# Performance work log

Hardware: AMD Instinct MI355X
Metric: run time of the kernel (lower is better)

The kernel has to match this reference:

```python
import jax, jax.numpy as jnp
import numpy as np

BN_EPS = 1e-5
N_EULER = 8


def _bn_train(x, gamma, beta):
    # BatchNorm1d in training mode: biased batch statistics over the batch axis
    mu = jnp.mean(x, axis=0)
    var = jnp.mean((x - mu) ** 2, axis=0)
    return gamma * (x - mu) / jnp.sqrt(var + BN_EPS) + beta


def setup_inputs() -> dict:
    key = jax.random.key(0)
    ks = jax.random.split(key, 16)
    B, d, u_dim, n_obs, sdim = 4096, 512, 64, 25, 128
    h1, h2, hd = 1024, 1024, 512

    def w(k, shape, fan_in):
        return jax.random.normal(k, shape, dtype=jnp.float32) / np.sqrt(fan_in)

    return {
        "z_dyn": jax.random.normal(ks[0], (B, d), dtype=jnp.float32),
        "z_static": jax.random.normal(ks[1], (B, sdim), dtype=jnp.float32),
        "dt": jnp.array(0.05, dtype=jnp.float32),
        "ut": jax.random.normal(ks[2], (B, u_dim), dtype=jnp.float32),
        "eps": jax.random.normal(ks[3], (N_EULER, B, d), dtype=jnp.float32),
        "W1": w(ks[4], (h1, d), d), "b1": jnp.zeros((h1,), jnp.float32),
        "g1": jnp.ones((h1,), jnp.float32), "be1": jnp.zeros((h1,), jnp.float32),
        "W2": w(ks[5], (h2, h1), h1), "b2": jnp.zeros((h2,), jnp.float32),
        "g2": jnp.ones((h2,), jnp.float32), "be2": jnp.zeros((h2,), jnp.float32),
        "W3": w(ks[6], (d, h2), h2), "b3": jnp.zeros((d,), jnp.float32),
        "Wd1": w(ks[7], (hd, d), d), "bd1": jnp.zeros((hd,), jnp.float32),
        "Wd2": w(ks[8], (d, hd), hd), "bd2": jnp.zeros((d,), jnp.float32),
        "B_sde": w(ks[9], (d, u_dim), u_dim),
        "C": w(ks[10], (n_obs, d), d),
        "D": w(ks[11], (n_obs, u_dim), u_dim),
    }


def reference(z_dyn, z_static, dt, ut, eps,
              W1, b1, g1, be1, W2, b2, g2, be2, W3, b3,
              Wd1, bd1, Wd2, bd2, B_sde, C, D):
    h = dt / N_EULER
    sqrt_h = jnp.sqrt(jnp.abs(h) + 1e-8)

    def drift(z):
        a = jax.nn.relu(_bn_train(z @ W1.T + b1, g1, be1))
        a = jax.nn.relu(_bn_train(a @ W2.T + b2, g2, be2))
        return a @ W3.T + b3

    def diffusion(z):
        t = jnp.tanh(z @ Wd1.T + bd1)
        return jax.nn.softplus(t @ Wd2.T + bd2) + 1e-5

    def step(z, e):
        f = drift(z)
        g = diffusion(z)
        z = z + h * f + sqrt_h * g * e  # Euler-Maruyama update (training mode)
        return z, None

    z, _ = jax.lax.scan(step, z_dyn, eps)
    ut_dt = ut * dt
    z_next = z + ut_dt @ B_sde.T
    yt = z_next @ C.T + ut_dt @ D.T
    return (z_next, yt)
```

## Files before the change

### kernel.cpp

```cpp
#include <hip/hip_runtime.h>


typedef unsigned short ushort_t;
typedef __bf16 bf16x8 __attribute__((ext_vector_type(8)));
typedef float f32x4 __attribute__((ext_vector_type(4)));

__device__ __forceinline__ float bf2f(ushort_t s) {
  unsigned u = ((unsigned)s) << 16;
  return __uint_as_float(u);
}
__device__ __forceinline__ ushort_t f2bf(float f) {
  unsigned u = __float_as_uint(f);
  unsigned lsb = (u >> 16) & 1u;
  u += 0x7fffu + lsb;
  return (ushort_t)(u >> 16);
}
__device__ __forceinline__ float ldin(const void* p, size_t i, int f32) {
  return f32 ? ((const float*)p)[i] : bf2f(((const ushort_t*)p)[i]);
}
__device__ __forceinline__ void async16(const void* g, void* l) {
  __builtin_amdgcn_global_load_lds(
      (const __attribute__((address_space(1))) void*)g,
      (__attribute__((address_space(3))) void*)l, 16, 0, 0);
}

__global__ void k_detect(const void* __restrict__ eps, const void* __restrict__ dtraw,
                         float* __restrict__ consts) {
  __shared__ float mx[256];
  const int t = threadIdx.x;
  const ushort_t* e = (const ushort_t*)eps;
  float m = 0.f;
#pragma unroll
  for (int k = 0; k < 4; ++k) {
    float v = fabsf(bf2f(e[t * 4 + k]));
    if (!(v < 1e30f)) v = 1e30f;
    m = fmaxf(m, v);
  }
  mx[t] = m;
  __syncthreads();
  if (t == 0) {
    float M = 0.f;
    for (int k = 0; k < 256; ++k) M = fmaxf(M, mx[k]);
    const int f32 = (M > 1e3f) ? 1 : 0;
    float dt;
    if (f32) {
      dt = *(const float*)dtraw;
    } else {
      float db = bf2f(*(const ushort_t*)dtraw);
      float df = *(const float*)dtraw;
      dt = (db > 1e-6f && db < 1e3f) ? db : df;
    }
    const float h = dt * 0.125f;
    consts[0] = h;
    consts[1] = sqrtf(fabsf(h) + 1e-8f);
    consts[2] = dt;
    consts[3] = (float)f32;
  }
}

struct ConvArgs { const void* src[5]; };
#define CONV_TOT 2621440

__global__ void k_conv(ConvArgs a, const float* __restrict__ consts,
                       ushort_t* __restrict__ base) {
  constexpr int CUM[6] = {0, 524288, 786432, 1835008, 2359296, 2621440};
  const int f32 = consts[3] != 0.f;
  const int i = (blockIdx.x * 256 + threadIdx.x) * 4;
  if (i >= CONV_TOT) return;
  int j = 0;
#pragma unroll
  for (int k = 1; k < 5; ++k)
    if (i >= CUM[k]) j = k;
  const int local = i - CUM[j];
  const void* s = a.src[j];
  ushort4 o;
  if (f32) {
    float4 v = ((const float4*)s)[local >> 2];
    o = make_ushort4(f2bf(v.x), f2bf(v.y), f2bf(v.z), f2bf(v.w));
  } else {
    o = ((const ushort4*)s)[local >> 2];
  }
  *(ushort4*)(base + i) = o;
}

template <int MT, int MODE, int STATS, int FUSE, int BIAS, int FINAL, int ANORM>
__device__ __forceinline__ void gemm_body(
    const ushort_t* __restrict__ A, const ushort_t* __restrict__ W,
    const void* __restrict__ bias, int ncol0, ushort_t* __restrict__ Cout,
    int Nout, int K, int m0, int n0, __bf16* As, __bf16* Bs,
    float* __restrict__ s1, float* __restrict__ s2,
    const ushort_t* __restrict__ Gb, float* __restrict__ zf,
    ushort_t* __restrict__ zb, const void* __restrict__ eps,
    unsigned long long eoff, const float* __restrict__ consts,
    const float* __restrict__ Ub, float* __restrict__ out0,
    const float* __restrict__ s1in, const float* __restrict__ s2in,
    const void* __restrict__ gsc, const void* __restrict__ gbe,
    float* scF, float* shF) {
  constexpr int BM = MT * 64;
  const int f32 = consts[3] != 0.f;
  const int tid = threadIdx.x;
  const int lane = tid & 63;
  const int wave = tid >> 6;
  const int col = lane & 15;
  const int quad = lane >> 4;
  const int rowBase = wave * (BM / 4);

  if (ANORM) {
    const float inv = 1.0f / 4096.0f;
    for (int c = tid; c < K; c += 256) {
      float mu = s1in[c] * inv;
      float var = fmaxf(s2in[c] * inv - mu * mu, 0.f);
      float sc = ldin(gsc, c, f32) * rsqrtf(var + 1e-5f);
      scF[c] = sc;
      shF[c] = ldin(gbe, c, f32) - mu * sc;
    }
  }

  f32x4 acc[MT][4] = {};

  for (int k0 = 0; k0 < K; k0 += 64) {
#pragma unroll
    for (int j = 0; j < BM / 32; ++j) {
      int chunk = j * 256 + tid;
      int row = chunk >> 3;
      int kc = chunk & 7;
      async16(A + (size_t)(m0 + row) * K + k0 + kc * 8, (char*)As + chunk * 16);
    }
#pragma unroll
    for (int j = 0; j < 2; ++j) {
      int chunk = j * 256 + tid;
      int row = chunk >> 3;
      int kc = chunk & 7;
      async16(W + (size_t)(n0 + row) * K + k0 + kc * 8, (char*)Bs + chunk * 16);
    }
    __syncthreads();

#pragma unroll
    for (int kk = 0; kk < 2; ++kk) {
      const int kb = kk * 32 + quad * 8;
      bf16x8 af[MT], bfr[4];
      if (ANORM) {
        float sc8[8], sh8[8];
        *(float4*)&sc8[0] = *(const float4*)&scF[k0 + kb];
        *(float4*)&sc8[4] = *(const float4*)&scF[k0 + kb + 4];
        *(float4*)&sh8[0] = *(const float4*)&shF[k0 + kb];
        *(float4*)&sh8[4] = *(const float4*)&shF[k0 + kb + 4];
#pragma unroll
        for (int mt = 0; mt < MT; ++mt) {
          bf16x8 raw = *(const bf16x8*)&As[(rowBase + mt * 16 + col) * 64 + kb];
#pragma unroll
          for (int j = 0; j < 8; ++j)
            af[mt][j] =
                (__bf16)fmaxf(fmaf((float)raw[j], sc8[j], sh8[j]), 0.f);
        }
      } else {
#pragma unroll
        for (int mt = 0; mt < MT; ++mt)
          af[mt] = *(const bf16x8*)&As[(rowBase + mt * 16 + col) * 64 + kb];
      }
#pragma unroll
      for (int nt = 0; nt < 4; ++nt)
        bfr[nt] = *(const bf16x8*)&Bs[(nt * 16 + col) * 64 + kb];
#pragma unroll
      for (int mt = 0; mt < MT; ++mt)
#pragma unroll
        for (int nt = 0; nt < 4; ++nt)
          acc[mt][nt] = __builtin_amdgcn_mfma_f32_16x16x32_bf16(
              af[mt], bfr[nt], acc[mt][nt], 0, 0, 0);
    }
    __syncthreads();
  }

  float* sS = (float*)As;
  float* sQ = (float*)As + 64;
  if (STATS) {
    if (tid < 128) ((float*)As)[tid] = 0.f;
    __syncthreads();
  }

  const float h = consts[0], sh = consts[1];

#pragma unroll
  for (int nt = 0; nt < 4; ++nt) {
    const int gn = n0 + nt * 16 + col;
    const float bv = BIAS ? ldin(bias, gn + ncol0, f32) : 0.f;
    float ls = 0.f, lq = 0.f;
#pragma unroll
    for (int mt = 0; mt < MT; ++mt) {
#pragma unroll
      for (int r = 0; r < 4; ++r) {
        const int gm = m0 + rowBase + mt * 16 + quad * 4 + r;
        float v = acc[mt][nt][r] + bv;
        if (STATS) {
          ls += v;
          lq += v * v;
        }
        if (MODE == 1) {
          v = tanhf(v);
        } else if (MODE == 2) {
          v = fmaxf(v, 0.f) + log1pf(expf(-fabsf(v))) + 1e-5f;
        }
        const size_t o = (size_t)gm * Nout + gn + ncol0;
        if (FUSE) {
          const float e = ldin(eps, eoff + o, f32);
          const float g = bf2f(Gb[o]);
          const float z = zf[o] + h * v + sh * g * e;
          zf[o] = z;
          zb[o] = f2bf(z);
          if (FINAL) out0[o] = z + Ub[o];
        } else {
          Cout[o] = f2bf(v);
        }
      }
    }
    if (STATS) {
      atomicAdd(&sS[nt * 16 + col], ls);
      atomicAdd(&sQ[nt * 16 + col], lq);
    }
  }

  if (STATS) {
    __syncthreads();
    if (tid < 64) {
      atomicAdd(&s1[n0 + tid], sS[tid]);
      atomicAdd(&s2[n0 + tid], sQ[tid]);
    }
  }
}

__global__ __launch_bounds__(256, 3) void k_x1t(
    const ushort_t* __restrict__ zb, const ushort_t* __restrict__ Wcat,
    const void* __restrict__ bd1, ushort_t* __restrict__ Xb,
    ushort_t* __restrict__ Tb, float* __restrict__ s1, float* __restrict__ s2,
    const float* __restrict__ consts) {
  __shared__ __bf16 As[128 * 64] __attribute__((aligned(16)));
  __shared__ __bf16 Bs[64 * 64] __attribute__((aligned(16)));
  const int L = blockIdx.x;
  const int q = L & 7, w = L >> 3;
  const int mloc = w & 3, n = w >> 2;
  const int m0 = (q * 4 + mloc) * 128;
  const int n0 = n * 64;
  if (n < 16) {
    gemm_body<2, 0, 1, 0, 0, 0, 0>(zb, Wcat, nullptr, 0, Xb, 1024, 512, m0, n0,
                                   As, Bs, s1, s2, nullptr, nullptr, nullptr,
                                   nullptr, 0, consts, nullptr, nullptr,
                                   nullptr, nullptr, nullptr, nullptr,
                                   nullptr, nullptr);
  } else {
    gemm_body<2, 1, 0, 0, 1, 0, 0>(zb, Wcat, bd1, -1024, Tb, 512, 512, m0, n0,
                                   As, Bs, nullptr, nullptr, nullptr, nullptr,
                                   nullptr, nullptr, 0, consts, nullptr,
                                   nullptr, nullptr, nullptr, nullptr, nullptr,
                                   nullptr, nullptr);
  }
}

__global__ __launch_bounds__(256, 3) void k_x2g(
    const ushort_t* __restrict__ X1raw, const ushort_t* __restrict__ W2c,
    const ushort_t* __restrict__ Tb, const ushort_t* __restrict__ Wd2c,
    const void* __restrict__ bd2, ushort_t* __restrict__ Ab,
    ushort_t* __restrict__ Gb, float* __restrict__ s1o, float* __restrict__ s2o,
    const float* __restrict__ s1i, const float* __restrict__ s2i,
    const void* __restrict__ g1, const void* __restrict__ be1,
    const float* __restrict__ consts) {
  __shared__ __bf16 As[128 * 64] __attribute__((aligned(16)));
  __shared__ __bf16 Bs[64 * 64] __attribute__((aligned(16)));
  __shared__ float scF[1024], shF[1024];
  const int L = blockIdx.x;
  if (L < 512) {
    const int q = L & 7, w = L >> 3;
    const int mloc = w & 3, n = w >> 2;
    const int m0 = (q * 4 + mloc) * 128, n0 = n * 64;
    gemm_body<2, 0, 1, 0, 0, 0, 1>(X1raw, W2c, nullptr, 0, Ab, 1024, 1024, m0,
                                   n0, As, Bs, s1o, s2o, nullptr, nullptr,
                                   nullptr, nullptr, 0, consts, nullptr,
                                   nullptr, s1i, s2i, g1, be1, scF, shF);
  } else {
    const int Lg = L - 512;
    const int q = Lg & 7, w = Lg >> 3;
    const int mloc = w & 7, n = w >> 3;
    const int m0 = (q * 8 + mloc) * 64, n0 = n * 64;
    gemm_body<1, 2, 0, 0, 1, 0, 0>(Tb, Wd2c, bd2, 0, Gb, 512, 512, m0, n0,
                                   As, Bs, nullptr, nullptr, nullptr, nullptr,
                                   nullptr, nullptr, 0, consts, nullptr,
                                   nullptr, nullptr, nullptr, nullptr, nullptr,
                                   nullptr, nullptr);
  }
}

template <int FINAL>
__global__ __launch_bounds__(256, 4) void k_fupd(
    const ushort_t* __restrict__ X2raw, const ushort_t* __restrict__ W3c,
    const void* __restrict__ b3, const ushort_t* __restrict__ Gb,
    float* __restrict__ zf, ushort_t* __restrict__ zb,
    const void* __restrict__ eps, unsigned long long eoff,
    const float* __restrict__ consts, const float* __restrict__ Ub,
    float* __restrict__ out0, const float* __restrict__ s1i,
    const float* __restrict__ s2i, const void* __restrict__ g2,
    const void* __restrict__ be2) {
  __shared__ __bf16 As[64 * 64] __attribute__((aligned(16)));
  __shared__ __bf16 Bs[64 * 64] __attribute__((aligned(16)));
  __shared__ float scF[1024], shF[1024];
  const int L = blockIdx.x;
  const int q = L & 7, w = L >> 3;
  const int mloc = w & 7, n = w >> 3;
  const int m0 = (q * 8 + mloc) * 64, n0 = n * 64;
  gemm_body<1, 0, 0, 1, 1, FINAL, 1>(X2raw, W3c, b3, 0, nullptr, 512, 1024,
                                     m0, n0, As, Bs, nullptr, nullptr, Gb, zf,
                                     zb, eps, eoff, consts, Ub, out0, s1i,
                                     s2i, g2, be2, scF, shF);
}

__global__ void k_init(const void* __restrict__ z, float* __restrict__ zf,
                       ushort_t* __restrict__ zb, const float* __restrict__ consts) {
  const int f32 = consts[3] != 0.f;
  const int i = blockIdx.x * 256 + threadIdx.x;
  float4 v;
  if (f32) {
    v = ((const float4*)z)[i];
  } else {
    ushort4 u = ((const ushort4*)z)[i];
    v = make_float4(bf2f(u.x), bf2f(u.y), bf2f(u.z), bf2f(u.w));
  }
  ((float4*)zf)[i] = v;
  ((ushort4*)zb)[i] = make_ushort4(f2bf(v.x), f2bf(v.y), f2bf(v.z), f2bf(v.w));
}

__global__ __launch_bounds__(256) void k_ub(
    const void* __restrict__ ut, const void* __restrict__ Bsde,
    const float* __restrict__ consts, float* __restrict__ Ub) {
  __shared__ float As[64][68];
  __shared__ float Bs[64][68];
  const float dt = consts[2];
  const int f32 = consts[3] != 0.f;
  const int t = threadIdx.x;
  const int tx = t & 15, ty = t >> 4;
  const int n0 = blockIdx.x * 64, m0 = blockIdx.y * 64;
  const int r = t >> 2;
  const int c0 = (t & 3) * 16;

#pragma unroll
  for (int j = 0; j < 16; ++j) {
    As[c0 + j][r] = ldin(ut, (size_t)(m0 + r) * 64 + c0 + j, f32);
    Bs[c0 + j][r] = ldin(Bsde, (size_t)(n0 + r) * 64 + c0 + j, f32);
  }
  __syncthreads();

  float acc[4][4] = {};
#pragma unroll 8
  for (int kk = 0; kk < 64; ++kk) {
    float a[4], b[4];
    *(float4*)a = *(const float4*)&As[kk][ty * 4];
    *(float4*)b = *(const float4*)&Bs[kk][tx * 4];
#pragma unroll
    for (int i = 0; i < 4; ++i)
#pragma unroll
      for (int j = 0; j < 4; ++j) acc[i][j] += a[i] * b[j];
  }

#pragma unroll
  for (int i = 0; i < 4; ++i) {
    const size_t o = (size_t)(m0 + ty * 4 + i) * 512 + n0 + tx * 4;
    *(float4*)&Ub[o] = make_float4(dt * acc[i][0], dt * acc[i][1],
                                   dt * acc[i][2], dt * acc[i][3]);
  }
}

__global__ void k_deff(const void* __restrict__ Cm, const void* __restrict__ Bsde,
                       const void* __restrict__ Dm, const float* __restrict__ consts,
                       float* __restrict__ Deff) {
  __shared__ float red[4][64];
  const int f32 = consts[3] != 0.f;
  const int j = blockIdx.x;
  const int k = threadIdx.x & 63;
  const int part = threadIdx.x >> 6;
  float acc = 0.f;
  const int l0 = part * 128;
#pragma unroll 8
  for (int l = l0; l < l0 + 128; ++l)
    acc += ldin(Cm, (size_t)j * 512 + l, f32) * ldin(Bsde, (size_t)l * 64 + k, f32);
  red[part][k] = acc;
  __syncthreads();
  if (part == 0) {
    float s = red[0][k] + red[1][k] + red[2][k] + red[3][k];
    Deff[j * 64 + k] = s + ldin(Dm, (size_t)j * 64 + k, f32);
  }
}

__global__ __launch_bounds__(256) void k_final2(
    const float* __restrict__ zf, const void* __restrict__ ut,
    const float* __restrict__ consts, const void* __restrict__ Cm,
    const float* __restrict__ Deff, float* __restrict__ out1) {
  const float dt = consts[2];
  const int f32 = consts[3] != 0.f;
  const int t = threadIdx.x;
  const int lane = t & 63;
  const int m = blockIdx.x * 4 + (t >> 6);
  float z8[8];
#pragma unroll
  for (int i = 0; i < 8; ++i) z8[i] = zf[(size_t)m * 512 + i * 64 + lane];
  const float u = ldin(ut, (size_t)m * 64 + lane, f32);

  for (int j = 0; j < 25; ++j) {
    float p = dt * u * Deff[j * 64 + lane];
#pragma unroll
    for (int i = 0; i < 8; ++i)
      p += z8[i] * ldin(Cm, (size_t)j * 512 + i * 64 + lane, f32);
#pragma unroll
    for (int off = 32; off > 0; off >>= 1) p += __shfl_down(p, off, 64);
    if (lane == 0) out1[m * 25 + j] = p;
  }
}

extern "C" void kernel_launch(void* const* d_in, const int* in_sizes, int n_in,
                              void* d_out, int out_size, void* d_ws, size_t ws_size,
                              hipStream_t stream) {
  static const int expA[22] = {
      2097152, 524288, 1,      262144, 16777216, 524288, 1024, 1024,
      1024,    1048576, 1024,  1024,   1024,     524288, 512,  262144,
      512,     262144, 512,    32768,  12800,    1600};

  int map[21];
  bool okA = (n_in == 22), okB = (n_in == 21);
  if (okA)
    for (int i = 0; i < 22; ++i)
      if (in_sizes[i] != expA[i]) { okA = false; break; }
  if (okB) {
    int j = 0;
    for (int i = 0; i < 22; ++i) {
      if (i == 1) continue;
      if (in_sizes[j] != expA[i]) { okB = false; break; }
      ++j;
    }
  }
  if (okA) {
    map[0] = 0;
    for (int i = 1; i < 21; ++i) map[i] = i + 1;
  } else if (okB) {
    for (int i = 0; i < 21; ++i) map[i] = i;
  } else {
    map[0] = 0;
    for (int i = 1; i < 21; ++i) map[i] = (i + 1 < n_in) ? i + 1 : n_in - 1;
  }

  const void* z_dyn = d_in[map[0]];
  const void* dtp = d_in[map[1]];
  const void* ut = d_in[map[2]];
  const void* eps = d_in[map[3]];
  const void* W1 = d_in[map[4]];
  const void* g1 = d_in[map[6]];
  const void* be1 = d_in[map[7]];
  const void* W2 = d_in[map[8]];
  const void* g2 = d_in[map[10]];
  const void* be2 = d_in[map[11]];
  const void* W3 = d_in[map[12]];
  const void* b3 = d_in[map[13]];
  const void* Wd1 = d_in[map[14]];
  const void* bd1 = d_in[map[15]];
  const void* Wd2 = d_in[map[16]];
  const void* bd2 = d_in[map[17]];
  const void* Bsde = d_in[map[18]];
  const void* Cm = d_in[map[19]];
  const void* Dm = d_in[map[20]];

  char* ws = (char*)d_ws;
  const size_t MB = 1024 * 1024;
  float* zf = (float*)(ws + 0);
  ushort_t* zb = (ushort_t*)(ws + 8 * MB);
  ushort_t* Xb = (ushort_t*)(ws + 12 * MB);
  ushort_t* Ab = (ushort_t*)(ws + 20 * MB);
  ushort_t* Tb = (ushort_t*)(ws + 28 * MB);
  ushort_t* Gb = (ushort_t*)(ws + 32 * MB);
  float* Ub = (float*)(ws + 36 * MB);
  ushort_t* canon = (ushort_t*)(ws + 44 * MB);
  float* stats = (float*)(ws + 49 * MB + 512 * 1024);
  float* consts = stats + 16 * 2048;
  float* Deff = consts + 16;

  const ushort_t* Wcat = canon + 0;
  const ushort_t* W2c = canon + 786432;
  const ushort_t* W3c = canon + 1835008;
  const ushort_t* Wd2c = canon + 2359296;

  float* out_z = (float*)d_out;
  float* out_y = out_z + 4096 * 512;

  const dim3 blk(256);

  k_detect<<<1, blk, 0, stream>>>(eps, dtp, consts);

  ConvArgs ca;
  ca.src[0] = W1;
  ca.src[1] = Wd1;
  ca.src[2] = W2;
  ca.src[3] = W3;
  ca.src[4] = Wd2;
  k_conv<<<(CONV_TOT / 4 + 255) / 256, blk, 0, stream>>>(ca, consts, canon);

  hipMemsetAsync(stats, 0, 16 * 2048 * sizeof(float), stream);
  k_init<<<2048, blk, 0, stream>>>(z_dyn, zf, zb, consts);
  k_ub<<<dim3(8, 64), blk, 0, stream>>>(ut, Bsde, consts, Ub);
  k_deff<<<25, blk, 0, stream>>>(Cm, Bsde, Dm, consts, Deff);

  for (int s = 0; s < 8; ++s) {
    float* sA1 = stats + (s * 2 + 0) * 2048;
    float* sA2 = stats + (s * 2 + 1) * 2048;
    const unsigned long long eoff = (unsigned long long)s * 4096 * 512;

    k_x1t<<<768, blk, 0, stream>>>(zb, Wcat, bd1, Xb, Tb,
                                   sA1, sA1 + 1024, consts);

    k_x2g<<<1024, blk, 0, stream>>>(Xb, W2c, Tb, Wd2c, bd2, Ab, Gb,
                                    sA2, sA2 + 1024, sA1, sA1 + 1024,
                                    g1, be1, consts);

    if (s < 7) {
      k_fupd<0><<<512, blk, 0, stream>>>(Ab, W3c, b3, Gb, zf, zb, eps, eoff,
                                         consts, Ub, out_z, sA2, sA2 + 1024,
                                         g2, be2);
    } else {
      k_fupd<1><<<512, blk, 0, stream>>>(Ab, W3c, b3, Gb, zf, zb, eps, eoff,
                                         consts, Ub, out_z, sA2, sA2 + 1024,
                                         g2, be2);
    }
  }

  k_final2<<<1024, blk, 0, stream>>>(zf, ut, consts, Cm, Deff, out_y);
}
```

Baseline: 884.1 us.

## Load MFMA operands directly from global memory, bypassing LDS staging

The GEMM body no longer stages A and W tiles in shared memory with async global-to-LDS loads and barriers. Each lane now reads its bf16x8 fragments straight from global memory. K becomes a template constant so the k-loop can be fully unrolled. The intent is to remove LDS traffic and per-tile __syncthreads. The cost is redundant global/L2 reads of W across waves, less coalesced 16-byte row-strided accesses, and larger code and register pressure from the unrolling.

Result: slower. 1.462 ms (+65.4%).

```diff
diff --git a/kernel.cpp b/kernel.cpp
--- a/kernel.cpp
+++ b/kernel.cpp
@@ -17,11 +17,6 @@
 }
 __device__ __forceinline__ float ldin(const void* p, size_t i, int f32) {
   return f32 ? ((const float*)p)[i] : bf2f(((const ushort_t*)p)[i]);
-}
-__device__ __forceinline__ void async16(const void* g, void* l) {
-  __builtin_amdgcn_global_load_lds(
-      (const __attribute__((address_space(1))) void*)g,
-      (__attribute__((address_space(3))) void*)l, 16, 0, 0);
 }
 
 __global__ void k_detect(const void* __restrict__ eps, const void* __restrict__ dtraw,
@@ -83,98 +78,85 @@
   *(ushort4*)(base + i) = o;
 }
 
-template <int MT, int MODE, int STATS, int FUSE, int BIAS, int FINAL, int ANORM>
+template <int MT, int KTOT, int MODE, int STATS, int FUSE, int BIAS, int FINAL,
+          int ANORM>
 __device__ __forceinline__ void gemm_body(
     const ushort_t* __restrict__ A, const ushort_t* __restrict__ W,
     const void* __restrict__ bias, int ncol0, ushort_t* __restrict__ Cout,
-    int Nout, int K, int m0, int n0, __bf16* As, __bf16* Bs,
-    float* __restrict__ s1, float* __restrict__ s2,
+    int Nout, int m0, int n0, float* __restrict__ s1, float* __restrict__ s2,
     const ushort_t* __restrict__ Gb, float* __restrict__ zf,
     ushort_t* __restrict__ zb, const void* __restrict__ eps,
     unsigned long long eoff, const float* __restrict__ consts,
     const float* __restrict__ Ub, float* __restrict__ out0,
     const float* __restrict__ s1in, const float* __restrict__ s2in,
     const void* __restrict__ gsc, const void* __restrict__ gbe,
-    float* scF, float* shF) {
-  constexpr int BM = MT * 64;
+    float* scF, float* shF, float* sS) {
   const int f32 = consts[3] != 0.f;
   const int tid = threadIdx.x;
   const int lane = tid & 63;
   const int wave = tid >> 6;
   const int col = lane & 15;
   const int quad = lane >> 4;
-  const int rowBase = wave * (BM / 4);
+  const int rowBase = wave * (MT * 16);
 
   if (ANORM) {
     const float inv = 1.0f / 4096.0f;
-    for (int c = tid; c < K; c += 256) {
+    for (int c = tid; c < KTOT; c += 256) {
       float mu = s1in[c] * inv;
       float var = fmaxf(s2in[c] * inv - mu * mu, 0.f);
       float sc = ldin(gsc, c, f32) * rsqrtf(var + 1e-5f);
       scF[c] = sc;
       shF[c] = ldin(gbe, c, f32) - mu * sc;
     }
-  }
+    __syncthreads();
+  }
+
+  const ushort_t* baseA[MT];
+#pragma unroll
+  for (int mt = 0; mt < MT; ++mt)
+    baseA[mt] = A + (size_t)(m0 + rowBase + mt * 16 + col) * KTOT + quad * 8;
+  const ushort_t* baseB[4];
+#pragma unroll
+  for (int nt = 0; nt < 4; ++nt)
+    baseB[nt] = W + (size_t)(n0 + nt * 16 + col) * KTOT + quad * 8;
 
   f32x4 acc[MT][4] = {};
 
-  for (int k0 = 0; k0 < K; k0 += 64) {
-#pragma unroll
-    for (int j = 0; j < BM / 32; ++j) {
-      int chunk = j * 256 + tid;
-      int row = chunk >> 3;
-      int kc = chunk & 7;
-      async16(A + (size_t)(m0 + row) * K + k0 + kc * 8, (char*)As + chunk * 16);
-    }
-#pragma unroll
-    for (int j = 0; j < 2; ++j) {
-      int chunk = j * 256 + tid;
-      int row = chunk >> 3;
-      int kc = chunk & 7;
-      async16(W + (size_t)(n0 + row) * K + k0 + kc * 8, (char*)Bs + chunk * 16);
-    }
-    __syncthreads();
-
-#pragma unroll
-    for (int kk = 0; kk < 2; ++kk) {
-      const int kb = kk * 32 + quad * 8;
-      bf16x8 af[MT], bfr[4];
-      if (ANORM) {
-        float sc8[8], sh8[8];
-        *(float4*)&sc8[0] = *(const float4*)&scF[k0 + kb];
-        *(float4*)&sc8[4] = *(const float4*)&scF[k0 + kb + 4];
-        *(float4*)&sh8[0] = *(const float4*)&shF[k0 + kb];
-        *(float4*)&sh8[4] = *(const float4*)&shF[k0 + kb + 4];
-#pragma unroll
-        for (int mt = 0; mt < MT; ++mt) {
-          bf16x8 raw = *(const bf16x8*)&As[(rowBase + mt * 16 + col) * 64 + kb];
-#pragma unroll
-          for (int j = 0; j < 8; ++j)
-            af[mt][j] =
-                (__bf16)fmaxf(fmaf((float)raw[j], sc8[j], sh8[j]), 0.f);
-        }
-      } else {
-#pragma unroll
-        for (int mt = 0; mt < MT; ++mt)
-          af[mt] = *(const bf16x8*)&As[(rowBase + mt * 16 + col) * 64 + kb];
+#pragma unroll
+  for (int k0 = 0; k0 < KTOT; k0 += 32) {
+    bf16x8 af[MT], bfr[4];
+#pragma unroll
+    for (int mt = 0; mt < MT; ++mt)
+      af[mt] = *(const bf16x8*)(baseA[mt] + k0);
+#pragma unroll
+    for (int nt = 0; nt < 4; ++nt)
+      bfr[nt] = *(const bf16x8*)(baseB[nt] + k0);
+    if (ANORM) {
+      float sc8[8], sh8[8];
+      const int kb = k0 + quad * 8;
+      *(float4*)&sc8[0] = *(const float4*)&scF[kb];
+      *(float4*)&sc8[4] = *(const float4*)&scF[kb + 4];
+      *(float4*)&sh8[0] = *(const float4*)&shF[kb];
+      *(float4*)&sh8[4] = *(const float4*)&shF[kb + 4];
+#pragma unroll
+      for (int mt = 0; mt < MT; ++mt) {
+#pragma unroll
+        for (int j = 0; j < 8; ++j)
+          af[mt][j] =
+              (__bf16)fmaxf(fmaf((float)af[mt][j], sc8[j], sh8[j]), 0.f);
       }
+    }
+#pragma unroll
+    for (int mt = 0; mt < MT; ++mt)
 #pragma unroll
       for (int nt = 0; nt < 4; ++nt)
-        bfr[nt] = *(const bf16x8*)&Bs[(nt * 16 + col) * 64 + kb];
-#pragma unroll
-      for (int mt = 0; mt < MT; ++mt)
-#pragma unroll
-        for (int nt = 0; nt < 4; ++nt)
-          acc[mt][nt] = __builtin_amdgcn_mfma_f32_16x16x32_bf16(
-              af[mt], bfr[nt], acc[mt][nt], 0, 0, 0);
-    }
-    __syncthreads();
-  }
-
-  float* sS = (float*)As;
-  float* sQ = (float*)As + 64;
+        acc[mt][nt] = __builtin_amdgcn_mfma_f32_16x16x32_bf16(
+            af[mt], bfr[nt], acc[mt][nt], 0, 0, 0);
+  }
+
+  float* sQ = sS + 64;
   if (STATS) {
-    if (tid < 128) ((float*)As)[tid] = 0.f;
+    if (tid < 128) sS[tid] = 0.f;
     __syncthreads();
   }
 
@@ -233,25 +215,22 @@
     const void* __restrict__ bd1, ushort_t* __restrict__ Xb,
     ushort_t* __restrict__ Tb, float* __restrict__ s1, float* __restrict__ s2,
     const float* __restrict__ consts) {
-  __shared__ __bf16 As[128 * 64] __attribute__((aligned(16)));
-  __shared__ __bf16 Bs[64 * 64] __attribute__((aligned(16)));
+  __shared__ float sS[128];
   const int L = blockIdx.x;
   const int q = L & 7, w = L >> 3;
   const int mloc = w & 3, n = w >> 2;
   const int m0 = (q * 4 + mloc) * 128;
   const int n0 = n * 64;
   if (n < 16) {
-    gemm_body<2, 0, 1, 0, 0, 0, 0>(zb, Wcat, nullptr, 0, Xb, 1024, 512, m0, n0,
-                                   As, Bs, s1, s2, nullptr, nullptr, nullptr,
-                                   nullptr, 0, consts, nullptr, nullptr,
-                                   nullptr, nullptr, nullptr, nullptr,
-                                   nullptr, nullptr);
+    gemm_body<2, 512, 0, 1, 0, 0, 0, 0>(
+        zb, Wcat, nullptr, 0, Xb, 1024, m0, n0, s1, s2, nullptr, nullptr,
+        nullptr, nullptr, 0, consts, nullptr, nullptr, nullptr, nullptr,
+        nullptr, nullptr, nullptr, nullptr, sS);
   } else {
-    gemm_body<2, 1, 0, 0, 1, 0, 0>(zb, Wcat, bd1, -1024, Tb, 512, 512, m0, n0,
-                                   As, Bs, nullptr, nullptr, nullptr, nullptr,
-                                   nullptr, nullptr, 0, consts, nullptr,
-                                   nullptr, nullptr, nullptr, nullptr, nullptr,
-                                   nullptr, nullptr);
+    gemm_body<2, 512, 1, 0, 0, 1, 0, 0>(
+        zb, Wcat, bd1, -1024, Tb, 512, m0, n0, nullptr, nullptr, nullptr,
+        nullptr, nullptr, nullptr, 0, consts, nullptr, nullptr, nullptr,
+        nullptr, nullptr, nullptr, nullptr, nullptr, sS);
   }
 }
 
@@ -263,28 +242,26 @@
     const float* __restrict__ s1i, const float* __restrict__ s2i,
     const void* __restrict__ g1, const void* __restrict__ be1,
     const float* __restrict__ consts) {
-  __shared__ __bf16 As[128 * 64] __attribute__((aligned(16)));
-  __shared__ __bf16 Bs[64 * 64] __attribute__((aligned(16)));
   __shared__ float scF[1024], shF[1024];
+  __shared__ float sS[128];
   const int L = blockIdx.x;
   if (L < 512) {
     const int q = L & 7, w = L >> 3;
     const int mloc = w & 3, n = w >> 2;
     const int m0 = (q * 4 + mloc) * 128, n0 = n * 64;
-    gemm_body<2, 0, 1, 0, 0, 0, 1>(X1raw, W2c, nullptr, 0, Ab, 1024, 1024, m0,
-                                   n0, As, Bs, s1o, s2o, nullptr, nullptr,
-                                   nullptr, nullptr, 0, consts, nullptr,
-                                   nullptr, s1i, s2i, g1, be1, scF, shF);
+    gemm_body<2, 1024, 0, 1, 0, 0, 0, 1>(
+        X1raw, W2c, nullptr, 0, Ab, 1024, m0, n0, s1o, s2o, nullptr, nullptr,
+        nullptr, nullptr, 0, consts, nullptr, nullptr, s1i, s2i, g1, be1, scF,
+        shF, sS);
   } else {
     const int Lg = L - 512;
     const int q = Lg & 7, w = Lg >> 3;
     const int mloc = w & 7, n = w >> 3;
     const int m0 = (q * 8 + mloc) * 64, n0 = n * 64;
-    gemm_body<1, 2, 0, 0, 1, 0, 0>(Tb, Wd2c, bd2, 0, Gb, 512, 512, m0, n0,
-                                   As, Bs, nullptr, nullptr, nullptr, nullptr,
-                                   nullptr, nullptr, 0, consts, nullptr,
-                                   nullptr, nullptr, nullptr, nullptr, nullptr,
-                                   nullptr, nullptr);
+    gemm_body<1, 512, 2, 0, 0, 1, 0, 0>(
+        Tb, Wd2c, bd2, 0, Gb, 512, m0, n0, nullptr, nullptr, nullptr, nullptr,
+        nullptr, nullptr, 0, consts, nullptr, nullptr, nullptr, nullptr,
+        nullptr, nullptr, nullptr, nullptr, sS);
   }
 }
 
@@ -298,17 +275,14 @@
     float* __restrict__ out0, const float* __restrict__ s1i,
     const float* __restrict__ s2i, const void* __restrict__ g2,
     const void* __restrict__ be2) {
-  __shared__ __bf16 As[64 * 64] __attribute__((aligned(16)));
-  __shared__ __bf16 Bs[64 * 64] __attribute__((aligned(16)));
   __shared__ float scF[1024], shF[1024];
   const int L = blockIdx.x;
   const int q = L & 7, w = L >> 3;
   const int mloc = w & 7, n = w >> 3;
   const int m0 = (q * 8 + mloc) * 64, n0 = n * 64;
-  gemm_body<1, 0, 0, 1, 1, FINAL, 1>(X2raw, W3c, b3, 0, nullptr, 512, 1024,
-                                     m0, n0, As, Bs, nullptr, nullptr, Gb, zf,
-                                     zb, eps, eoff, consts, Ub, out0, s1i,
-                                     s2i, g2, be2, scF, shF);
+  gemm_body<1, 1024, 0, 0, 1, 1, FINAL, 1>(
+      X2raw, W3c, b3, 0, nullptr, 512, m0, n0, nullptr, nullptr, Gb, zf, zb,
+      eps, eoff, consts, Ub, out0, s1i, s2i, g2, be2, scF, shF, nullptr);
 }
 
 __global__ void k_init(const void* __restrict__ z, float* __restrict__ zf,
```

## Widen GEMM N-tiles to 128 and XOR-swizzle LDS fragment layout

Applied to the files above, without the earlier changes.

Adds an NT template parameter so each block computes a 128-wide output tile instead of 64, halving grid sizes for the x1t, x2g and fupd kernels and raising A-tile reuse per block. It also XOR-swizzles the 16-byte chunks written to LDS by the async loads and reads them back through a matching lds_frag helper, to avoid LDS bank conflicts on fragment reads. The cost is more accumulators and LDS per block, so launch bounds drop to 2 blocks per SM, and the smaller grids (256–384 blocks) may leave compute units underused.

Result: slower. 943.8 us (+6.8%).

```diff
diff --git a/kernel.cpp b/kernel.cpp
--- a/kernel.cpp
+++ b/kernel.cpp
@@ -22,6 +22,11 @@
   __builtin_amdgcn_global_load_lds(
       (const __attribute__((address_space(1))) void*)g,
       (__attribute__((address_space(3))) void*)l, 16, 0, 0);
+}
+
+__device__ __forceinline__ bf16x8 lds_frag(const __bf16* T, int row, int kb) {
+  const int byte = (row << 7) + ((((kb >> 3) ^ (row & 7))) << 4);
+  return *(const bf16x8*)((const char*)T + byte);
 }
 
 __global__ void k_detect(const void* __restrict__ eps, const void* __restrict__ dtraw,
@@ -83,7 +88,8 @@
   *(ushort4*)(base + i) = o;
 }
 
-template <int MT, int MODE, int STATS, int FUSE, int BIAS, int FINAL, int ANORM>
+template <int MT, int NT, int MODE, int STATS, int FUSE, int BIAS, int FINAL,
+          int ANORM>
 __device__ __forceinline__ void gemm_body(
     const ushort_t* __restrict__ A, const ushort_t* __restrict__ W,
     const void* __restrict__ bias, int ncol0, ushort_t* __restrict__ Cout,
@@ -95,15 +101,16 @@
     const float* __restrict__ Ub, float* __restrict__ out0,
     const float* __restrict__ s1in, const float* __restrict__ s2in,
     const void* __restrict__ gsc, const void* __restrict__ gbe,
-    float* scF, float* shF) {
+    float* scF, float* shF, float* sS) {
   constexpr int BM = MT * 64;
+  constexpr int BN = NT * 16;
   const int f32 = consts[3] != 0.f;
   const int tid = threadIdx.x;
   const int lane = tid & 63;
   const int wave = tid >> 6;
   const int col = lane & 15;
   const int quad = lane >> 4;
-  const int rowBase = wave * (BM / 4);
+  const int rowBase = wave * (MT * 16);
 
   if (ANORM) {
     const float inv = 1.0f / 4096.0f;
@@ -116,7 +123,7 @@
     }
   }
 
-  f32x4 acc[MT][4] = {};
+  f32x4 acc[MT][NT] = {};
 
   for (int k0 = 0; k0 < K; k0 += 64) {
 #pragma unroll
@@ -124,21 +131,23 @@
       int chunk = j * 256 + tid;
       int row = chunk >> 3;
       int kc = chunk & 7;
-      async16(A + (size_t)(m0 + row) * K + k0 + kc * 8, (char*)As + chunk * 16);
-    }
-#pragma unroll
-    for (int j = 0; j < 2; ++j) {
+      async16(A + (size_t)(m0 + row) * K + k0 + ((kc ^ (row & 7)) << 3),
+              (char*)As + chunk * 16);
+    }
+#pragma unroll
+    for (int j = 0; j < BN / 32; ++j) {
       int chunk = j * 256 + tid;
       int row = chunk >> 3;
       int kc = chunk & 7;
-      async16(W + (size_t)(n0 + row) * K + k0 + kc * 8, (char*)Bs + chunk * 16);
+      async16(W + (size_t)(n0 + row) * K + k0 + ((kc ^ (row & 7)) << 3),
+              (char*)Bs + chunk * 16);
     }
     __syncthreads();
 
 #pragma unroll
     for (int kk = 0; kk < 2; ++kk) {
       const int kb = kk * 32 + quad * 8;
-      bf16x8 af[MT], bfr[4];
+      bf16x8 af[MT], bfr[NT];
       if (ANORM) {
         float sc8[8], sh8[8];
         *(float4*)&sc8[0] = *(const float4*)&scF[k0 + kb];
@@ -147,7 +156,7 @@
         *(float4*)&sh8[4] = *(const float4*)&shF[k0 + kb + 4];
 #pragma unroll
         for (int mt = 0; mt < MT; ++mt) {
-          bf16x8 raw = *(const bf16x8*)&As[(rowBase + mt * 16 + col) * 64 + kb];
+          bf16x8 raw = lds_frag(As, rowBase + mt * 16 + col, kb);
 #pragma unroll
           for (int j = 0; j < 8; ++j)
             af[mt][j] =
@@ -156,32 +165,30 @@
       } else {
 #pragma unroll
         for (int mt = 0; mt < MT; ++mt)
-          af[mt] = *(const bf16x8*)&As[(rowBase + mt * 16 + col) * 64 + kb];
+          af[mt] = lds_frag(As, rowBase + mt * 16 + col, kb);
       }
 #pragma unroll
-      for (int nt = 0; nt < 4; ++nt)
-        bfr[nt] = *(const bf16x8*)&Bs[(nt * 16 + col) * 64 + kb];
+      for (int nt = 0; nt < NT; ++nt)
+        bfr[nt] = lds_frag(Bs, nt * 16 + col, kb);
 #pragma unroll
       for (int mt = 0; mt < MT; ++mt)
 #pragma unroll
-        for (int nt = 0; nt < 4; ++nt)
+        for (int nt = 0; nt < NT; ++nt)
           acc[mt][nt] = __builtin_amdgcn_mfma_f32_16x16x32_bf16(
               af[mt], bfr[nt], acc[mt][nt], 0, 0, 0);
     }
     __syncthreads();
   }
 
-  float* sS = (float*)As;
-  float* sQ = (float*)As + 64;
   if (STATS) {
-    if (tid < 128) ((float*)As)[tid] = 0.f;
+    for (int i = tid; i < 2 * BN; i += 256) sS[i] = 0.f;
     __syncthreads();
   }
 
   const float h = consts[0], sh = consts[1];
 
 #pragma unroll
-  for (int nt = 0; nt < 4; ++nt) {
+  for (int nt = 0; nt < NT; ++nt) {
     const int gn = n0 + nt * 16 + col;
     const float bv = BIAS ? ldin(bias, gn + ncol0, f32) : 0.f;
     float ls = 0.f, lq = 0.f;
@@ -215,47 +222,46 @@
     }
     if (STATS) {
       atomicAdd(&sS[nt * 16 + col], ls);
-      atomicAdd(&sQ[nt * 16 + col], lq);
+      atomicAdd(&sS[BN + nt * 16 + col], lq);
     }
   }
 
   if (STATS) {
     __syncthreads();
-    if (tid < 64) {
+    if (tid < BN) {
       atomicAdd(&s1[n0 + tid], sS[tid]);
-      atomicAdd(&s2[n0 + tid], sQ[tid]);
-    }
-  }
-}
-
-__global__ __launch_bounds__(256, 3) void k_x1t(
+      atomicAdd(&s2[n0 + tid], sS[BN + tid]);
+    }
+  }
+}
+
+__global__ __launch_bounds__(256, 2) void k_x1t(
     const ushort_t* __restrict__ zb, const ushort_t* __restrict__ Wcat,
     const void* __restrict__ bd1, ushort_t* __restrict__ Xb,
     ushort_t* __restrict__ Tb, float* __restrict__ s1, float* __restrict__ s2,
     const float* __restrict__ consts) {
   __shared__ __bf16 As[128 * 64] __attribute__((aligned(16)));
-  __shared__ __bf16 Bs[64 * 64] __attribute__((aligned(16)));
+  __shared__ __bf16 Bs[128 * 64] __attribute__((aligned(16)));
+  __shared__ float sS[256];
   const int L = blockIdx.x;
   const int q = L & 7, w = L >> 3;
   const int mloc = w & 3, n = w >> 2;
   const int m0 = (q * 4 + mloc) * 128;
-  const int n0 = n * 64;
-  if (n < 16) {
-    gemm_body<2, 0, 1, 0, 0, 0, 0>(zb, Wcat, nullptr, 0, Xb, 1024, 512, m0, n0,
-                                   As, Bs, s1, s2, nullptr, nullptr, nullptr,
-                                   nullptr, 0, consts, nullptr, nullptr,
-                                   nullptr, nullptr, nullptr, nullptr,
-                                   nullptr, nullptr);
+  const int n0 = n * 128;
+  if (n < 8) {
+    gemm_body<2, 8, 0, 1, 0, 0, 0, 0>(
+        zb, Wcat, nullptr, 0, Xb, 1024, 512, m0, n0, As, Bs, s1, s2, nullptr,
+        nullptr, nullptr, nullptr, 0, consts, nullptr, nullptr, nullptr,
+        nullptr, nullptr, nullptr, nullptr, nullptr, sS);
   } else {
-    gemm_body<2, 1, 0, 0, 1, 0, 0>(zb, Wcat, bd1, -1024, Tb, 512, 512, m0, n0,
-                                   As, Bs, nullptr, nullptr, nullptr, nullptr,
-                                   nullptr, nullptr, 0, consts, nullptr,
-                                   nullptr, nullptr, nullptr, nullptr, nullptr,
-                                   nullptr, nullptr);
-  }
-}
-
-__global__ __launch_bounds__(256, 3) void k_x2g(
+    gemm_body<2, 8, 1, 0, 0, 1, 0, 0>(
+        zb, Wcat, bd1, -1024, Tb, 512, 512, m0, n0, As, Bs, nullptr, nullptr,
+        nullptr, nullptr, nullptr, nullptr, 0, consts, nullptr, nullptr,
+        nullptr, nullptr, nullptr, nullptr, nullptr, nullptr, sS);
+  }
+}
+
+__global__ __launch_bounds__(256, 2) void k_x2g(
     const ushort_t* __restrict__ X1raw, const ushort_t* __restrict__ W2c,
     const ushort_t* __restrict__ Tb, const ushort_t* __restrict__ Wd2c,
     const void* __restrict__ bd2, ushort_t* __restrict__ Ab,
@@ -264,32 +270,32 @@
     const void* __restrict__ g1, const void* __restrict__ be1,
     const float* __restrict__ consts) {
   __shared__ __bf16 As[128 * 64] __attribute__((aligned(16)));
-  __shared__ __bf16 Bs[64 * 64] __attribute__((aligned(16)));
+  __shared__ __bf16 Bs[128 * 64] __attribute__((aligned(16)));
   __shared__ float scF[1024], shF[1024];
+  __shared__ float sS[256];
   const int L = blockIdx.x;
-  if (L < 512) {
+  if (L < 256) {
     const int q = L & 7, w = L >> 3;
     const int mloc = w & 3, n = w >> 2;
-    const int m0 = (q * 4 + mloc) * 128, n0 = n * 64;
-    gemm_body<2, 0, 1, 0, 0, 0, 1>(X1raw, W2c, nullptr, 0, Ab, 1024, 1024, m0,
-                                   n0, As, Bs, s1o, s2o, nullptr, nullptr,
-                                   nullptr, nullptr, 0, consts, nullptr,
-                                   nullptr, s1i, s2i, g1, be1, scF, shF);
+    const int m0 = (q * 4 + mloc) * 128, n0 = n * 128;
+    gemm_body<2, 8, 0, 1, 0, 0, 0, 1>(
+        X1raw, W2c, nullptr, 0, Ab, 1024, 1024, m0, n0, As, Bs, s1o, s2o,
+        nullptr, nullptr, nullptr, nullptr, 0, consts, nullptr, nullptr, s1i,
+        s2i, g1, be1, scF, shF, sS);
   } else {
-    const int Lg = L - 512;
+    const int Lg = L - 256;
     const int q = Lg & 7, w = Lg >> 3;
-    const int mloc = w & 7, n = w >> 3;
-    const int m0 = (q * 8 + mloc) * 64, n0 = n * 64;
-    gemm_body<1, 2, 0, 0, 1, 0, 0>(Tb, Wd2c, bd2, 0, Gb, 512, 512, m0, n0,
-                                   As, Bs, nullptr, nullptr, nullptr, nullptr,
-                                   nullptr, nullptr, 0, consts, nullptr,
-                                   nullptr, nullptr, nullptr, nullptr, nullptr,
-                                   nullptr, nullptr);
+    const int mloc = w & 3, n = w >> 2;
+    const int m0 = (q * 4 + mloc) * 128, n0 = n * 128;
+    gemm_body<2, 8, 2, 0, 0, 1, 0, 0>(
+        Tb, Wd2c, bd2, 0, Gb, 512, 512, m0, n0, As, Bs, nullptr, nullptr,
+        nullptr, nullptr, nullptr, nullptr, 0, consts, nullptr, nullptr,
+        nullptr, nullptr, nullptr, nullptr, nullptr, nullptr, sS);
   }
 }
 
 template <int FINAL>
-__global__ __launch_bounds__(256, 4) void k_fupd(
+__global__ __launch_bounds__(256, 2) void k_fupd(
     const ushort_t* __restrict__ X2raw, const ushort_t* __restrict__ W3c,
     const void* __restrict__ b3, const ushort_t* __restrict__ Gb,
     float* __restrict__ zf, ushort_t* __restrict__ zb,
@@ -299,16 +305,16 @@
     const float* __restrict__ s2i, const void* __restrict__ g2,
     const void* __restrict__ be2) {
   __shared__ __bf16 As[64 * 64] __attribute__((aligned(16)));
-  __shared__ __bf16 Bs[64 * 64] __attribute__((aligned(16)));
+  __shared__ __bf16 Bs[128 * 64] __attribute__((aligned(16)));
   __shared__ float scF[1024], shF[1024];
   const int L = blockIdx.x;
   const int q = L & 7, w = L >> 3;
   const int mloc = w & 7, n = w >> 3;
-  const int m0 = (q * 8 + mloc) * 64, n0 = n * 64;
-  gemm_body<1, 0, 0, 1, 1, FINAL, 1>(X2raw, W3c, b3, 0, nullptr, 512, 1024,
-                                     m0, n0, As, Bs, nullptr, nullptr, Gb, zf,
-                                     zb, eps, eoff, consts, Ub, out0, s1i,
-                                     s2i, g2, be2, scF, shF);
+  const int m0 = (q * 8 + mloc) * 64, n0 = n * 128;
+  gemm_body<1, 8, 0, 0, 1, 1, FINAL, 1>(
+      X2raw, W3c, b3, 0, nullptr, 512, 1024, m0, n0, As, Bs, nullptr, nullptr,
+      Gb, zf, zb, eps, eoff, consts, Ub, out0, s1i, s2i, g2, be2, scF, shF,
+      nullptr);
 }
 
 __global__ void k_init(const void* __restrict__ z, float* __restrict__ zf,
@@ -507,19 +513,19 @@
     float* sA2 = stats + (s * 2 + 1) * 2048;
     const unsigned long long eoff = (unsigned long long)s * 4096 * 512;
 
-    k_x1t<<<768, blk, 0, stream>>>(zb, Wcat, bd1, Xb, Tb,
+    k_x1t<<<384, blk, 0, stream>>>(zb, Wcat, bd1, Xb, Tb,
                                    sA1, sA1 + 1024, consts);
 
-    k_x2g<<<1024, blk, 0, stream>>>(Xb, W2c, Tb, Wd2c, bd2, Ab, Gb,
-                                    sA2, sA2 + 1024, sA1, sA1 + 1024,
-                                    g1, be1, consts);
+    k_x2g<<<384, blk, 0, stream>>>(Xb, W2c, Tb, Wd2c, bd2, Ab, Gb,
+                                   sA2, sA2 + 1024, sA1, sA1 + 1024,
+                                   g1, be1, consts);
 
     if (s < 7) {
-      k_fupd<0><<<512, blk, 0, stream>>>(Ab, W3c, b3, Gb, zf, zb, eps, eoff,
+      k_fupd<0><<<256, blk, 0, stream>>>(Ab, W3c, b3, Gb, zf, zb, eps, eoff,
                                          consts, Ub, out_z, sA2, sA2 + 1024,
                                          g2, be2);
     } else {
-      k_fupd<1><<<512, blk, 0, stream>>>(Ab, W3c, b3, Gb, zf, zb, eps, eoff,
+      k_fupd<1><<<256, blk, 0, stream>>>(Ab, W3c, b3, Gb, zf, zb, eps, eoff,
                                          consts, Ub, out_z, sA2, sA2 + 1024,
                                          g2, be2);
     }
```

## Double-buffer LDS tiles and XOR-swizzle layout in shared GEMM body

Applied to the files above, without the earlier changes.

The GEMM main loop now double-buffers the A and B tiles in LDS, issuing async global-to-LDS loads for the next K slice while MFMAs run on the current one. That removes one barrier per iteration. Tile rows are also stored with an XOR swizzle of the 16-byte chunk index to cut LDS bank conflicts on fragment reads. The cost is twice the LDS footprint, which lowers occupancy (k_x2g launch bounds drop from 3 to 2 blocks). The BN stats scratch moves to its own shared array.

Result: faster. 840.9 us (-4.9%).

```diff
diff --git a/kernel.cpp b/kernel.cpp
--- a/kernel.cpp
+++ b/kernel.cpp
@@ -22,6 +22,11 @@
   __builtin_amdgcn_global_load_lds(
       (const __attribute__((address_space(1))) void*)g,
       (__attribute__((address_space(3))) void*)l, 16, 0, 0);
+}
+
+__device__ __forceinline__ bf16x8 lds_frag(const __bf16* T, int row, int kb) {
+  const int byte = (row << 7) + ((((kb >> 3) ^ (row & 7))) << 4);
+  return *(const bf16x8*)((const char*)T + byte);
 }
 
 __global__ void k_detect(const void* __restrict__ eps, const void* __restrict__ dtraw,
@@ -95,7 +100,7 @@
     const float* __restrict__ Ub, float* __restrict__ out0,
     const float* __restrict__ s1in, const float* __restrict__ s2in,
     const void* __restrict__ gsc, const void* __restrict__ gbe,
-    float* scF, float* shF) {
+    float* scF, float* shF, float* sS) {
   constexpr int BM = MT * 64;
   const int f32 = consts[3] != 0.f;
   const int tid = threadIdx.x;
@@ -103,7 +108,7 @@
   const int wave = tid >> 6;
   const int col = lane & 15;
   const int quad = lane >> 4;
-  const int rowBase = wave * (BM / 4);
+  const int rowBase = wave * (MT * 16);
 
   if (ANORM) {
     const float inv = 1.0f / 4096.0f;
@@ -116,24 +121,43 @@
     }
   }
 
+  const int srow = tid >> 3;
+  const int skc = tid & 7;
+  auto stageA = [&](int k0, __bf16* dst) {
+#pragma unroll
+    for (int j = 0; j < BM / 32; ++j) {
+      const int row = j * 32 + srow;
+      async16(A + (size_t)(m0 + row) * K + k0 + (((skc ^ (row & 7))) << 3),
+              (char*)dst + (j * 256 + tid) * 16);
+    }
+  };
+  auto stageB = [&](int k0, __bf16* dst) {
+#pragma unroll
+    for (int j = 0; j < 2; ++j) {
+      const int row = j * 32 + srow;
+      async16(W + (size_t)(n0 + row) * K + k0 + (((skc ^ (row & 7))) << 3),
+              (char*)dst + (j * 256 + tid) * 16);
+    }
+  };
+
   f32x4 acc[MT][4] = {};
 
-  for (int k0 = 0; k0 < K; k0 += 64) {
-#pragma unroll
-    for (int j = 0; j < BM / 32; ++j) {
-      int chunk = j * 256 + tid;
-      int row = chunk >> 3;
-      int kc = chunk & 7;
-      async16(A + (size_t)(m0 + row) * K + k0 + kc * 8, (char*)As + chunk * 16);
-    }
-#pragma unroll
-    for (int j = 0; j < 2; ++j) {
-      int chunk = j * 256 + tid;
-      int row = chunk >> 3;
-      int kc = chunk & 7;
-      async16(W + (size_t)(n0 + row) * K + k0 + kc * 8, (char*)Bs + chunk * 16);
-    }
-    __syncthreads();
+  __bf16* Acur = As;
+  __bf16* Aalt = As + BM * 64;
+  __bf16* Bcur = Bs;
+  __bf16* Balt = Bs + 64 * 64;
+
+  stageA(0, Acur);
+  stageB(0, Bcur);
+  __syncthreads();
+
+  const int NIT = K / 64;
+  for (int it = 0; it < NIT; ++it) {
+    const int k0 = it * 64;
+    if (it + 1 < NIT) {
+      stageA(k0 + 64, Aalt);
+      stageB(k0 + 64, Balt);
+    }
 
 #pragma unroll
     for (int kk = 0; kk < 2; ++kk) {
@@ -147,7 +171,7 @@
         *(float4*)&sh8[4] = *(const float4*)&shF[k0 + kb + 4];
 #pragma unroll
         for (int mt = 0; mt < MT; ++mt) {
-          bf16x8 raw = *(const bf16x8*)&As[(rowBase + mt * 16 + col) * 64 + kb];
+          bf16x8 raw = lds_frag(Acur, rowBase + mt * 16 + col, kb);
 #pragma unroll
           for (int j = 0; j < 8; ++j)
             af[mt][j] =
@@ -156,11 +180,11 @@
       } else {
 #pragma unroll
         for (int mt = 0; mt < MT; ++mt)
-          af[mt] = *(const bf16x8*)&As[(rowBase + mt * 16 + col) * 64 + kb];
+          af[mt] = lds_frag(Acur, rowBase + mt * 16 + col, kb);
       }
 #pragma unroll
       for (int nt = 0; nt < 4; ++nt)
-        bfr[nt] = *(const bf16x8*)&Bs[(nt * 16 + col) * 64 + kb];
+        bfr[nt] = lds_frag(Bcur, nt * 16 + col, kb);
 #pragma unroll
       for (int mt = 0; mt < MT; ++mt)
 #pragma unroll
@@ -169,12 +193,12 @@
               af[mt], bfr[nt], acc[mt][nt], 0, 0, 0);
     }
     __syncthreads();
-  }
-
-  float* sS = (float*)As;
-  float* sQ = (float*)As + 64;
+    __bf16* t0 = Acur; Acur = Aalt; Aalt = t0;
+    __bf16* t1 = Bcur; Bcur = Balt; Balt = t1;
+  }
+
   if (STATS) {
-    if (tid < 128) ((float*)As)[tid] = 0.f;
+    for (int i = tid; i < 128; i += 256) sS[i] = 0.f;
     __syncthreads();
   }
 
@@ -215,7 +239,7 @@
     }
     if (STATS) {
       atomicAdd(&sS[nt * 16 + col], ls);
-      atomicAdd(&sQ[nt * 16 + col], lq);
+      atomicAdd(&sS[64 + nt * 16 + col], lq);
     }
   }
 
@@ -223,7 +247,7 @@
     __syncthreads();
     if (tid < 64) {
       atomicAdd(&s1[n0 + tid], sS[tid]);
-      atomicAdd(&s2[n0 + tid], sQ[tid]);
+      atomicAdd(&s2[n0 + tid], sS[64 + tid]);
     }
   }
 }
@@ -233,29 +257,28 @@
     const void* __restrict__ bd1, ushort_t* __restrict__ Xb,
     ushort_t* __restrict__ Tb, float* __restrict__ s1, float* __restrict__ s2,
     const float* __restrict__ consts) {
-  __shared__ __bf16 As[128 * 64] __attribute__((aligned(16)));
-  __shared__ __bf16 Bs[64 * 64] __attribute__((aligned(16)));
+  __shared__ __bf16 As[2 * 128 * 64] __attribute__((aligned(16)));
+  __shared__ __bf16 Bs[2 * 64 * 64] __attribute__((aligned(16)));
+  __shared__ float sS[128];
   const int L = blockIdx.x;
   const int q = L & 7, w = L >> 3;
   const int mloc = w & 3, n = w >> 2;
   const int m0 = (q * 4 + mloc) * 128;
   const int n0 = n * 64;
   if (n < 16) {
-    gemm_body<2, 0, 1, 0, 0, 0, 0>(zb, Wcat, nullptr, 0, Xb, 1024, 512, m0, n0,
-                                   As, Bs, s1, s2, nullptr, nullptr, nullptr,
-                                   nullptr, 0, consts, nullptr, nullptr,
-                                   nullptr, nullptr, nullptr, nullptr,
-                                   nullptr, nullptr);
+    gemm_body<2, 0, 1, 0, 0, 0, 0>(
+        zb, Wcat, nullptr, 0, Xb, 1024, 512, m0, n0, As, Bs, s1, s2, nullptr,
+        nullptr, nullptr, nullptr, 0, consts, nullptr, nullptr, nullptr,
+        nullptr, nullptr, nullptr, nullptr, nullptr, sS);
   } else {
-    gemm_body<2, 1, 0, 0, 1, 0, 0>(zb, Wcat, bd1, -1024, Tb, 512, 512, m0, n0,
-                                   As, Bs, nullptr, nullptr, nullptr, nullptr,
-                                   nullptr, nullptr, 0, consts, nullptr,
-                                   nullptr, nullptr, nullptr, nullptr, nullptr,
-                                   nullptr, nullptr);
-  }
-}
-
-__global__ __launch_bounds__(256, 3) void k_x2g(
+    gemm_body<2, 1, 0, 0, 1, 0, 0>(
+        zb, Wcat, bd1, -1024, Tb, 512, 512, m0, n0, As, Bs, nullptr, nullptr,
+        nullptr, nullptr, nullptr, nullptr, 0, consts, nullptr, nullptr,
+        nullptr, nullptr, nullptr, nullptr, nullptr, nullptr, sS);
+  }
+}
+
+__global__ __launch_bounds__(256, 2) void k_x2g(
     const ushort_t* __restrict__ X1raw, const ushort_t* __restrict__ W2c,
     const ushort_t* __restrict__ Tb, const ushort_t* __restrict__ Wd2c,
     const void* __restrict__ bd2, ushort_t* __restrict__ Ab,
@@ -263,28 +286,28 @@
     const float* __restrict__ s1i, const float* __restrict__ s2i,
     const void* __restrict__ g1, const void* __restrict__ be1,
     const float* __restrict__ consts) {
-  __shared__ __bf16 As[128 * 64] __attribute__((aligned(16)));
-  __shared__ __bf16 Bs[64 * 64] __attribute__((aligned(16)));
+  __shared__ __bf16 As[2 * 128 * 64] __attribute__((aligned(16)));
+  __shared__ __bf16 Bs[2 * 64 * 64] __attribute__((aligned(16)));
   __shared__ float scF[1024], shF[1024];
+  __shared__ float sS[128];
   const int L = blockIdx.x;
   if (L < 512) {
     const int q = L & 7, w = L >> 3;
     const int mloc = w & 3, n = w >> 2;
     const int m0 = (q * 4 + mloc) * 128, n0 = n * 64;
-    gemm_body<2, 0, 1, 0, 0, 0, 1>(X1raw, W2c, nullptr, 0, Ab, 1024, 1024, m0,
-                                   n0, As, Bs, s1o, s2o, nullptr, nullptr,
-                                   nullptr, nullptr, 0, consts, nullptr,
-                                   nullptr, s1i, s2i, g1, be1, scF, shF);
+    gemm_body<2, 0, 1, 0, 0, 0, 1>(
+        X1raw, W2c, nullptr, 0, Ab, 1024, 1024, m0, n0, As, Bs, s1o, s2o,
+        nullptr, nullptr, nullptr, nullptr, 0, consts, nullptr, nullptr, s1i,
+        s2i, g1, be1, scF, shF, sS);
   } else {
     const int Lg = L - 512;
     const int q = Lg & 7, w = Lg >> 3;
     const int mloc = w & 7, n = w >> 3;
     const int m0 = (q * 8 + mloc) * 64, n0 = n * 64;
-    gemm_body<1, 2, 0, 0, 1, 0, 0>(Tb, Wd2c, bd2, 0, Gb, 512, 512, m0, n0,
-                                   As, Bs, nullptr, nullptr, nullptr, nullptr,
-                                   nullptr, nullptr, 0, consts, nullptr,
-                                   nullptr, nullptr, nullptr, nullptr, nullptr,
-                                   nullptr, nullptr);
+    gemm_body<1, 2, 0, 0, 1, 0, 0>(
+        Tb, Wd2c, bd2, 0, Gb, 512, 512, m0, n0, As, Bs, nullptr, nullptr,
+        nullptr, nullptr, nullptr, nullptr, 0, consts, nullptr, nullptr,
+        nullptr, nullptr, nullptr, nullptr, nullptr, nullptr, sS);
   }
 }
 
@@ -298,17 +321,17 @@
     float* __restrict__ out0, const float* __restrict__ s1i,
     const float* __restrict__ s2i, const void* __restrict__ g2,
     const void* __restrict__ be2) {
-  __shared__ __bf16 As[64 * 64] __attribute__((aligned(16)));
-  __shared__ __bf16 Bs[64 * 64] __attribute__((aligned(16)));
+  __shared__ __bf16 As[2 * 64 * 64] __attribute__((aligned(16)));
+  __shared__ __bf16 Bs[2 * 64 * 64] __attribute__((aligned(16)));
   __shared__ float scF[1024], shF[1024];
   const int L = blockIdx.x;
   const int q = L & 7, w = L >> 3;
   const int mloc = w & 7, n = w >> 3;
   const int m0 = (q * 8 + mloc) * 64, n0 = n * 64;
-  gemm_body<1, 0, 0, 1, 1, FINAL, 1>(X2raw, W3c, b3, 0, nullptr, 512, 1024,
-                                     m0, n0, As, Bs, nullptr, nullptr, Gb, zf,
-                                     zb, eps, eoff, consts, Ub, out0, s1i,
-                                     s2i, g2, be2, scF, shF);
+  gemm_body<1, 0, 0, 1, 1, FINAL, 1>(
+      X2raw, W3c, b3, 0, nullptr, 512, 1024, m0, n0, As, Bs, nullptr, nullptr,
+      Gb, zf, zb, eps, eoff, consts, Ub, out0, s1i, s2i, g2, be2, scF, shF,
+      nullptr);
 }
 
 __global__ void k_init(const void* __restrict__ z, float* __restrict__ zf,
```
